# Kernel tuning notes

Measured on AMD Instinct MI355X. Metric: run time of the kernel, lower is better.

## Reference

```python
import jax, jax.numpy as jnp
import numpy as np

C_Z = 128
C_HIDDEN = 32
N_HEAD = 4
HC = N_HEAD * C_HIDDEN  # 128
LN_EPS = 1e-5


def setup_inputs() -> dict:
    key = jax.random.key(0)
    ks = jax.random.split(key, 8)
    b, n = 1, 256
    s = 1.0 / np.sqrt(C_Z)
    return {
        "z_ij": jax.random.normal(ks[0], (b, n, n, C_Z), dtype=jnp.float32),
        "ln_gamma": jnp.ones((C_Z,), dtype=jnp.float32),
        "ln_beta": jnp.zeros((C_Z,), dtype=jnp.float32),
        "Wq": jax.random.normal(ks[1], (C_Z, HC), dtype=jnp.float32) * s,
        "Wk": jax.random.normal(ks[2], (C_Z, HC), dtype=jnp.float32) * s,
        "Wv": jax.random.normal(ks[3], (C_Z, HC), dtype=jnp.float32) * s,
        "Wb": jax.random.normal(ks[4], (C_Z, N_HEAD), dtype=jnp.float32) * s,
        "Wg": jax.random.normal(ks[5], (C_Z, HC), dtype=jnp.float32) * s,
        "Wout": jax.random.normal(ks[6], (HC, C_Z), dtype=jnp.float32) * (1.0 / np.sqrt(HC)),
    }


def reference(z_ij, ln_gamma, ln_beta, Wq, Wk, Wv, Wb, Wg, Wout):
    b, n, _, _ = z_ij.shape
    # LayerNorm over c_z
    mu = jnp.mean(z_ij, axis=-1, keepdims=True)
    var = jnp.var(z_ij, axis=-1, keepdims=True)
    z = (z_ij - mu) * jax.lax.rsqrt(var + LN_EPS) * ln_gamma + ln_beta

    def heads(x):  # [b,i,j,hc] -> [b,i,j,h,d]
        return x.reshape(b, n, n, N_HEAD, C_HIDDEN)

    q = heads(z @ Wq)
    k = heads(z @ Wk)
    v = heads(z @ Wv)
    bias = z @ Wb                      # [b,i,j,h]
    g = jax.nn.sigmoid(heads(z @ Wg))  # [b,i,j,h,d]

    scores = jnp.einsum('bijhd,bikhd->bijkh', q, k) / np.sqrt(C_HIDDEN)
    scores = scores + bias[:, None]    # bias[b, j, k, h] broadcast over i
    a = jax.nn.softmax(scores, axis=-2)  # over k
    o = jnp.einsum('bijkh,bikhd->bijhd', a, v)
    o = (g * o).reshape(b, n, n, HC)
    return o @ Wout
```

## Files before the change

kernel.cpp:

```cpp
#include <hip/hip_runtime.h>

typedef _Float16 f16x8 __attribute__((ext_vector_type(8)));
typedef _Float16 f16x2 __attribute__((ext_vector_type(2)));
typedef float f32x4 __attribute__((ext_vector_type(4)));
typedef int i32x4 __attribute__((ext_vector_type(4)));

#define MFMA16(a, b, c) __builtin_amdgcn_mfma_f32_16x16x32_f16(a, b, c, 0, 0, 0)

#define NROW 65536
#define SEGB 16777216ull
#define LOG2E 1.4426950408889634f

__global__ __launch_bounds__(256) void k_ln(
    const float* __restrict__ z, const float* __restrict__ gamma,
    const float* __restrict__ beta, const float* __restrict__ Wb,
    const float* __restrict__ Wq, const float* __restrict__ Wk,
    const float* __restrict__ Wv, const float* __restrict__ Wg,
    const float* __restrict__ Wout,
    _Float16* __restrict__ zln, float* __restrict__ biasT,
    _Float16* __restrict__ WtAll)
{
  __shared__ _Float16 sw[32 * 136];
  int bid = blockIdx.x;
  if (bid < 16384) {
    int lane = threadIdx.x & 63;
    int w = threadIdx.x >> 6;
    int row = bid * 4 + w;
    float2 v = ((const float2*)(z + (size_t)row * 128))[lane];
    float s = v.x + v.y;
    #pragma unroll
    for (int m = 1; m < 64; m <<= 1) s += __shfl_xor(s, m);
    float mu = s * 0.0078125f;
    float dx = v.x - mu, dy = v.y - mu;
    float q = dx * dx + dy * dy;
    #pragma unroll
    for (int m = 1; m < 64; m <<= 1) q += __shfl_xor(q, m);
    float rs = rsqrtf(q * 0.0078125f + 1e-5f);
    float2 g2 = ((const float2*)gamma)[lane];
    float2 b2 = ((const float2*)beta)[lane];
    float y0 = dx * rs * g2.x + b2.x;
    float y1 = dy * rs * g2.y + b2.y;
    f16x2 pr; pr.x = (_Float16)y0; pr.y = (_Float16)y1;
    *(f16x2*)(zln + (size_t)row * 128 + 2 * lane) = pr;
    float4 wb0 = ((const float4*)Wb)[2 * lane];
    float4 wb1 = ((const float4*)Wb)[2 * lane + 1];
    float pb0 = y0 * wb0.x + y1 * wb1.x;
    float pb1 = y0 * wb0.y + y1 * wb1.y;
    float pb2 = y0 * wb0.z + y1 * wb1.z;
    float pb3 = y0 * wb0.w + y1 * wb1.w;
    #pragma unroll
    for (int m = 1; m < 64; m <<= 1) {
      pb0 += __shfl_xor(pb0, m);
      pb1 += __shfl_xor(pb1, m);
      pb2 += __shfl_xor(pb2, m);
      pb3 += __shfl_xor(pb3, m);
    }
    if (lane == 0) {
      int tix = ((row & 255) << 8) + (row >> 8);
      biasT[tix] = pb0 * LOG2E;
      biasT[NROW + tix] = pb1 * LOG2E;
      biasT[2 * NROW + tix] = pb2 * LOG2E;
      biasT[3 * NROW + tix] = pb3 * LOG2E;
    }
  } else {
    int t = bid - 16384;
    int mat = t >> 2, n0 = (t & 3) * 32;
    const float* src = (mat == 0) ? Wq : (mat == 1) ? Wk : (mat == 2) ? Wv
                       : (mat == 3) ? Wg : Wout;
    _Float16* dst = WtAll + mat * 16384;
    for (int it = 0; it < 16; ++it) {
      int e = threadIdx.x + it * 256;
      int c = e >> 5, j = e & 31;
      sw[j * 136 + c] = (_Float16)src[c * 128 + n0 + j];
    }
    __syncthreads();
    for (int it = 0; it < 2; ++it) {
      int ch = threadIdx.x + it * 256;
      int n = ch >> 4, k8 = (ch & 15) * 8;
      *(int4*)(dst + (n0 + n) * 128 + k8) = *(const int4*)&sw[n * 136 + k8];
    }
  }
}

__global__ __launch_bounds__(256) void k_proj(
    const _Float16* __restrict__ A, const _Float16* __restrict__ WtAll,
    _Float16* __restrict__ Qb, _Float16* __restrict__ Kb,
    _Float16* __restrict__ Vb, _Float16* __restrict__ Gb)
{
  __shared__ _Float16 sA[128 * 136];
  __shared__ _Float16 sB[128 * 136];
  int e = blockIdx.x;
  int by = (e >> 3) & 3;
  int xb = ((e >> 5) << 3) | (e & 7);
  int m0 = xb * 128;
  const _Float16* Bt = WtAll + by * 16384;
  _Float16* outp = (by == 0) ? Qb : (by == 1) ? Kb : (by == 2) ? Vb : Gb;
  int tid = threadIdx.x;
  for (int it = 0; it < 8; ++it) {
    int ch = tid + it * 256;
    int r = ch >> 4, c8 = (ch & 15) * 8;
    *(int4*)&sA[r * 136 + c8] = *(const int4*)(A + (size_t)(m0 + r) * 128 + c8);
    *(int4*)&sB[r * 136 + c8] = *(const int4*)(Bt + r * 128 + c8);
  }
  __syncthreads();
  int lane = tid & 63, w = tid >> 6;
  int mw = (w >> 1) * 64, nw = (w & 1) * 64;
  int lr = lane & 15, lg = lane >> 4;
  f32x4 z4 = {0.f, 0.f, 0.f, 0.f};
  f32x4 acc[4][4];
  #pragma unroll
  for (int mt = 0; mt < 4; ++mt)
    #pragma unroll
    for (int nt = 0; nt < 4; ++nt) acc[mt][nt] = z4;
  #pragma unroll
  for (int k0 = 0; k0 < 128; k0 += 32) {
    f16x8 af[4], bf[4];
    #pragma unroll
    for (int mt = 0; mt < 4; ++mt)
      af[mt] = *(const f16x8*)&sA[(mw + mt * 16 + lr) * 136 + k0 + lg * 8];
    #pragma unroll
    for (int nt = 0; nt < 4; ++nt)
      bf[nt] = *(const f16x8*)&sB[(nw + nt * 16 + lr) * 136 + k0 + lg * 8];
    #pragma unroll
    for (int mt = 0; mt < 4; ++mt)
      #pragma unroll
      for (int nt = 0; nt < 4; ++nt)
        acc[mt][nt] = MFMA16(af[mt], bf[nt], acc[mt][nt]);
  }
  bool sig = (by == 3);
  #pragma unroll
  for (int mt = 0; mt < 4; ++mt)
    #pragma unroll
    for (int nt = 0; nt < 4; ++nt)
      #pragma unroll
      for (int r = 0; r < 4; ++r) {
        int row = m0 + mw + mt * 16 + lg * 4 + r;
        int col = nw + nt * 16 + lr;
        float v = acc[mt][nt][r];
        if (sig) v = 1.0f / (1.0f + __expf(-v));
        outp[(size_t)row * 128 + col] = (_Float16)v;
      }
}

__global__ __launch_bounds__(256) void k_attn(
    const _Float16* __restrict__ Qb, const _Float16* __restrict__ Kb,
    const _Float16* __restrict__ Vb, const _Float16* __restrict__ Gb,
    const float* __restrict__ biasT, _Float16* __restrict__ OG)
{
  __shared__ _Float16 sK[256 * 32];
  __shared__ _Float16 sV[32 * 256];
  int i = blockIdx.x, h = blockIdx.y;
  int tid = threadIdx.x;
  size_t base = ((size_t)i * 256) * 128 + h * 32;
  for (int it = 0; it < 4; ++it) {
    int ch = tid + it * 256;
    int r = ch >> 2, cx = ch & 3;
    int p = cx ^ ((r >> 1) & 3);
    *(int4*)&sK[r * 32 + p * 8] = *(const int4*)(Kb + base + (size_t)r * 128 + cx * 8);
  }
  for (int it = 0; it < 4; ++it) {
    int ch = tid + it * 256;
    int k = ch >> 2, d8 = (ch & 3) * 8;
    f16x8 tv = *(const f16x8*)(Vb + base + (size_t)k * 128 + d8);
    #pragma unroll
    for (int jj = 0; jj < 8; ++jj) {
      int d = d8 + jj;
      int p = (k >> 3) ^ (d & 7);
      sV[d * 256 + p * 8 + (k & 7)] = tv[jj];
    }
  }
  __syncthreads();
  int lane = tid & 63, w = tid >> 6;
  int lr = lane & 15, lg = lane >> 4;
  const float scale = 0.2550348858f;
  f32x4 z4 = {0.f, 0.f, 0.f, 0.f};
  int la = lr + ((lg & 1) << 5);
  int lb = la + 16;
  int hi = lg >> 1;
  for (int pass = 0; pass < 4; ++pass) {
    int jbase = pass * 64;
    int jg = jbase + (w << 4) + lr;
    f16x8 aq = *(const f16x8*)(Qb + base + (size_t)jg * 128 + lg * 8);
    f32x4 sacc[16];
    __builtin_amdgcn_s_setprio(1);
    #pragma unroll
    for (int kt = 0; kt < 16; ++kt) {
      int r = kt * 16 + lr;
      int p = lg ^ ((r >> 1) & 3);
      f16x8 bk = *(const f16x8*)&sK[r * 32 + p * 8];
      sacc[kt] = MFMA16(bk, aq, z4);
    }
    __builtin_amdgcn_s_setprio(0);
    const float* bp = biasT + ((size_t)h << 16) + ((lg * 4) << 8) + jg;
    float mx = -1e30f;
    #pragma unroll
    for (int kt = 0; kt < 16; ++kt) {
      const float* bb = bp + (kt << 12);
      float b0 = bb[0], b1 = bb[256], b2 = bb[512], b3 = bb[768];
      sacc[kt][0] = sacc[kt][0] * scale + b0;
      sacc[kt][1] = sacc[kt][1] * scale + b1;
      sacc[kt][2] = sacc[kt][2] * scale + b2;
      sacc[kt][3] = sacc[kt][3] * scale + b3;
      mx = fmaxf(mx, fmaxf(fmaxf(sacc[kt][0], sacc[kt][1]),
                           fmaxf(sacc[kt][2], sacc[kt][3])));
    }
    mx = fmaxf(mx, __shfl_xor(mx, 16));
    mx = fmaxf(mx, __shfl_xor(mx, 32));
    float sum = 0.f;
    int q16[16][2];
    #pragma unroll
    for (int kt = 0; kt < 16; ++kt) {
      float p0 = exp2f(sacc[kt][0] - mx);
      float p1 = exp2f(sacc[kt][1] - mx);
      float p2 = exp2f(sacc[kt][2] - mx);
      float p3 = exp2f(sacc[kt][3] - mx);
      sum += (p0 + p1) + (p2 + p3);
      f16x2 w01, w23;
      w01.x = (_Float16)p0; w01.y = (_Float16)p1;
      w23.x = (_Float16)p2; w23.y = (_Float16)p3;
      q16[kt][0] = __builtin_bit_cast(int, w01);
      q16[kt][1] = __builtin_bit_cast(int, w23);
    }
    sum += __shfl_xor(sum, 16);
    sum += __shfl_xor(sum, 32);
    float rinv = 1.0f / sum;
    float rr0 = __shfl(rinv, (lg << 2));
    float rr1 = __shfl(rinv, (lg << 2) + 1);
    float rr2 = __shfl(rinv, (lg << 2) + 2);
    float rr3 = __shfl(rinv, (lg << 2) + 3);
    f32x4 oacc[2] = {z4, z4};
    #pragma unroll
    for (int ks = 0; ks < 8; ++ks) {
      int a0 = __shfl(q16[2 * ks][0], la);
      int a1 = __shfl(q16[2 * ks][1], la);
      int c0 = __shfl(q16[2 * ks + 1][0], la);
      int c1 = __shfl(q16[2 * ks + 1][1], la);
      int b0 = __shfl(q16[2 * ks][0], lb);
      int b1 = __shfl(q16[2 * ks][1], lb);
      int d0 = __shfl(q16[2 * ks + 1][0], lb);
      int d1 = __shfl(q16[2 * ks + 1][1], lb);
      i32x4 wv;
      wv.x = hi ? c0 : a0;
      wv.y = hi ? c1 : a1;
      wv.z = hi ? d0 : b0;
      wv.w = hi ? d1 : b1;
      f16x8 ap = __builtin_bit_cast(f16x8, wv);
      __builtin_amdgcn_s_setprio(1);
      #pragma unroll
      for (int nt = 0; nt < 2; ++nt) {
        int d = nt * 16 + lr;
        int c = ks * 4 + lg;
        f16x8 bv = *(const f16x8*)&sV[d * 256 + (c ^ (d & 7)) * 8];
        oacc[nt] = MFMA16(ap, bv, oacc[nt]);
      }
      __builtin_amdgcn_s_setprio(0);
    }
    float rrs[4] = {rr0, rr1, rr2, rr3};
    #pragma unroll
    for (int nt = 0; nt < 2; ++nt)
      #pragma unroll
      for (int r = 0; r < 4; ++r) {
        int j = jbase + (w << 4) + (lg << 2) + r;
        int d = nt * 16 + lr;
        size_t idx = base + (size_t)j * 128 + d;
        float g = (float)Gb[idx];
        OG[idx] = (_Float16)(oacc[nt][r] * rrs[r] * g);
      }
  }
}

__global__ __launch_bounds__(256) void k_outp(
    const _Float16* __restrict__ A, const _Float16* __restrict__ Bt,
    float* __restrict__ out)
{
  __shared__ _Float16 sA[128 * 136];
  __shared__ _Float16 sB[128 * 136];
  int m0 = blockIdx.x * 128;
  int tid = threadIdx.x;
  for (int it = 0; it < 8; ++it) {
    int ch = tid + it * 256;
    int r = ch >> 4, c8 = (ch & 15) * 8;
    *(int4*)&sA[r * 136 + c8] = *(const int4*)(A + (size_t)(m0 + r) * 128 + c8);
    *(int4*)&sB[r * 136 + c8] = *(const int4*)(Bt + r * 128 + c8);
  }
  __syncthreads();
  int lane = tid & 63, w = tid >> 6;
  int mw = (w >> 1) * 64, nw = (w & 1) * 64;
  int lr = lane & 15, lg = lane >> 4;
  f32x4 z4 = {0.f, 0.f, 0.f, 0.f};
  f32x4 acc[4][4];
  #pragma unroll
  for (int mt = 0; mt < 4; ++mt)
    #pragma unroll
    for (int nt = 0; nt < 4; ++nt) acc[mt][nt] = z4;
  #pragma unroll
  for (int k0 = 0; k0 < 128; k0 += 32) {
    f16x8 af[4], bf[4];
    #pragma unroll
    for (int mt = 0; mt < 4; ++mt)
      af[mt] = *(const f16x8*)&sA[(mw + mt * 16 + lr) * 136 + k0 + lg * 8];
    #pragma unroll
    for (int nt = 0; nt < 4; ++nt)
      bf[nt] = *(const f16x8*)&sB[(nw + nt * 16 + lr) * 136 + k0 + lg * 8];
    #pragma unroll
    for (int mt = 0; mt < 4; ++mt)
      #pragma unroll
      for (int nt = 0; nt < 4; ++nt)
        acc[mt][nt] = MFMA16(af[mt], bf[nt], acc[mt][nt]);
  }
  #pragma unroll
  for (int mt = 0; mt < 4; ++mt)
    #pragma unroll
    for (int nt = 0; nt < 4; ++nt)
      #pragma unroll
      for (int r = 0; r < 4; ++r) {
        int row = m0 + mw + mt * 16 + lg * 4 + r;
        int col = nw + nt * 16 + lr;
        out[(size_t)row * 128 + col] = acc[mt][nt][r];
      }
}

extern "C" void kernel_launch(void* const* d_in, const int* in_sizes, int n_in,
                              void* d_out, int out_size, void* d_ws, size_t ws_size,
                              hipStream_t stream) {
  (void)in_sizes; (void)n_in; (void)out_size; (void)ws_size;
  const float* z    = (const float*)d_in[0];
  const float* gam  = (const float*)d_in[1];
  const float* bet  = (const float*)d_in[2];
  const float* Wq   = (const float*)d_in[3];
  const float* Wk   = (const float*)d_in[4];
  const float* Wv   = (const float*)d_in[5];
  const float* Wb   = (const float*)d_in[6];
  const float* Wg   = (const float*)d_in[7];
  const float* Wout = (const float*)d_in[8];

  char* ws = (char*)d_ws;
  _Float16* zln   = (_Float16*)(ws);
  _Float16* Qb    = (_Float16*)(ws + SEGB);
  _Float16* Kb    = (_Float16*)(ws + SEGB * 2);
  _Float16* Vb    = (_Float16*)(ws + SEGB * 3);
  _Float16* Gb    = (_Float16*)(ws + SEGB * 4);
  float*    biasT = (float*)   (ws + SEGB * 5);
  _Float16* WtAll = (_Float16*)(ws + SEGB * 5 + 1048576);

  k_ln<<<16404, 256, 0, stream>>>(z, gam, bet, Wb, Wq, Wk, Wv, Wg, Wout,
                                  zln, biasT, WtAll);
  k_proj<<<2048, 256, 0, stream>>>(zln, WtAll, Qb, Kb, Vb, Gb);
  k_attn<<<dim3(256, 4), 256, 0, stream>>>(Qb, Kb, Vb, Gb, biasT, zln);
  k_outp<<<512, 256, 0, stream>>>(zln, WtAll + 4 * 16384, (float*)d_out);
}
```

Measured before the change: 215.0 us.

## Store bias untransposed for vector loads and interleave exp with PV MFMAs

The bias tensor is now written in natural row order, so the attention kernel reads four contiguous bias values per tile with one float4 load instead of four strided scalar loads. The softmax exponentials are also computed inside the PV MFMA loop rather than in a separate pass that materialised all sixteen packed probability pairs first. This cuts register pressure from the q16 array and lets transcendental work overlap with matrix instructions. The sum reduction still happens after the loop, so normalisation order is unchanged.

```diff
diff --git a/kernel.cpp b/kernel.cpp
--- a/kernel.cpp
+++ b/kernel.cpp
@@ -56,11 +56,10 @@
       pb3 += __shfl_xor(pb3, m);
     }
     if (lane == 0) {
-      int tix = ((row & 255) << 8) + (row >> 8);
-      biasT[tix] = pb0 * LOG2E;
-      biasT[NROW + tix] = pb1 * LOG2E;
-      biasT[2 * NROW + tix] = pb2 * LOG2E;
-      biasT[3 * NROW + tix] = pb3 * LOG2E;
+      biasT[row] = pb0 * LOG2E;
+      biasT[NROW + row] = pb1 * LOG2E;
+      biasT[2 * NROW + row] = pb2 * LOG2E;
+      biasT[3 * NROW + row] = pb3 * LOG2E;
     }
   } else {
     int t = bid - 16384;
@@ -191,35 +190,65 @@
       sacc[kt] = MFMA16(bk, aq, z4);
     }
     __builtin_amdgcn_s_setprio(0);
-    const float* bp = biasT + ((size_t)h << 16) + ((lg * 4) << 8) + jg;
+    const float* bp = biasT + ((size_t)h << 16) + ((size_t)jg << 8) + (lg << 2);
     float mx = -1e30f;
     #pragma unroll
     for (int kt = 0; kt < 16; ++kt) {
-      const float* bb = bp + (kt << 12);
-      float b0 = bb[0], b1 = bb[256], b2 = bb[512], b3 = bb[768];
-      sacc[kt][0] = sacc[kt][0] * scale + b0;
-      sacc[kt][1] = sacc[kt][1] * scale + b1;
-      sacc[kt][2] = sacc[kt][2] * scale + b2;
-      sacc[kt][3] = sacc[kt][3] * scale + b3;
+      float4 b4 = *(const float4*)(bp + kt * 16);
+      sacc[kt][0] = sacc[kt][0] * scale + b4.x;
+      sacc[kt][1] = sacc[kt][1] * scale + b4.y;
+      sacc[kt][2] = sacc[kt][2] * scale + b4.z;
+      sacc[kt][3] = sacc[kt][3] * scale + b4.w;
       mx = fmaxf(mx, fmaxf(fmaxf(sacc[kt][0], sacc[kt][1]),
                            fmaxf(sacc[kt][2], sacc[kt][3])));
     }
     mx = fmaxf(mx, __shfl_xor(mx, 16));
     mx = fmaxf(mx, __shfl_xor(mx, 32));
     float sum = 0.f;
-    int q16[16][2];
-    #pragma unroll
-    for (int kt = 0; kt < 16; ++kt) {
-      float p0 = exp2f(sacc[kt][0] - mx);
-      float p1 = exp2f(sacc[kt][1] - mx);
-      float p2 = exp2f(sacc[kt][2] - mx);
-      float p3 = exp2f(sacc[kt][3] - mx);
-      sum += (p0 + p1) + (p2 + p3);
-      f16x2 w01, w23;
-      w01.x = (_Float16)p0; w01.y = (_Float16)p1;
-      w23.x = (_Float16)p2; w23.y = (_Float16)p3;
-      q16[kt][0] = __builtin_bit_cast(int, w01);
-      q16[kt][1] = __builtin_bit_cast(int, w23);
+    f32x4 oacc[2] = {z4, z4};
+    #pragma unroll
+    for (int ks = 0; ks < 8; ++ks) {
+      float p0 = exp2f(sacc[2 * ks][0] - mx);
+      float p1 = exp2f(sacc[2 * ks][1] - mx);
+      float p2 = exp2f(sacc[2 * ks][2] - mx);
+      float p3 = exp2f(sacc[2 * ks][3] - mx);
+      float p4 = exp2f(sacc[2 * ks + 1][0] - mx);
+      float p5 = exp2f(sacc[2 * ks + 1][1] - mx);
+      float p6 = exp2f(sacc[2 * ks + 1][2] - mx);
+      float p7 = exp2f(sacc[2 * ks + 1][3] - mx);
+      sum += ((p0 + p1) + (p2 + p3)) + ((p4 + p5) + (p6 + p7));
+      f16x2 wA0, wA1, wB0, wB1;
+      wA0.x = (_Float16)p0; wA0.y = (_Float16)p1;
+      wA1.x = (_Float16)p2; wA1.y = (_Float16)p3;
+      wB0.x = (_Float16)p4; wB0.y = (_Float16)p5;
+      wB1.x = (_Float16)p6; wB1.y = (_Float16)p7;
+      int A0 = __builtin_bit_cast(int, wA0);
+      int A1 = __builtin_bit_cast(int, wA1);
+      int B0 = __builtin_bit_cast(int, wB0);
+      int B1 = __builtin_bit_cast(int, wB1);
+      int a0 = __shfl(A0, la);
+      int a1 = __shfl(A1, la);
+      int c0 = __shfl(B0, la);
+      int c1 = __shfl(B1, la);
+      int b0 = __shfl(A0, lb);
+      int b1 = __shfl(A1, lb);
+      int d0 = __shfl(B0, lb);
+      int d1 = __shfl(B1, lb);
+      i32x4 wv;
+      wv.x = hi ? c0 : a0;
+      wv.y = hi ? c1 : a1;
+      wv.z = hi ? d0 : b0;
+      wv.w = hi ? d1 : b1;
+      f16x8 ap = __builtin_bit_cast(f16x8, wv);
+      __builtin_amdgcn_s_setprio(1);
+      #pragma unroll
+      for (int nt = 0; nt < 2; ++nt) {
+        int d = nt * 16 + lr;
+        int c = ks * 4 + lg;
+        f16x8 bv = *(const f16x8*)&sV[d * 256 + (c ^ (d & 7)) * 8];
+        oacc[nt] = MFMA16(ap, bv, oacc[nt]);
+      }
+      __builtin_amdgcn_s_setprio(0);
     }
     sum += __shfl_xor(sum, 16);
     sum += __shfl_xor(sum, 32);
@@ -228,33 +257,6 @@
     float rr1 = __shfl(rinv, (lg << 2) + 1);
     float rr2 = __shfl(rinv, (lg << 2) + 2);
     float rr3 = __shfl(rinv, (lg << 2) + 3);
-    f32x4 oacc[2] = {z4, z4};
-    #pragma unroll
-    for (int ks = 0; ks < 8; ++ks) {
-      int a0 = __shfl(q16[2 * ks][0], la);
-      int a1 = __shfl(q16[2 * ks][1], la);
-      int c0 = __shfl(q16[2 * ks + 1][0], la);
-      int c1 = __shfl(q16[2 * ks + 1][1], la);
-      int b0 = __shfl(q16[2 * ks][0], lb);
-      int b1 = __shfl(q16[2 * ks][1], lb);
-      int d0 = __shfl(q16[2 * ks + 1][0], lb);
-      int d1 = __shfl(q16[2 * ks + 1][1], lb);
-      i32x4 wv;
-      wv.x = hi ? c0 : a0;
-      wv.y = hi ? c1 : a1;
-      wv.z = hi ? d0 : b0;
-      wv.w = hi ? d1 : b1;
-      f16x8 ap = __builtin_bit_cast(f16x8, wv);
-      __builtin_amdgcn_s_setprio(1);
-      #pragma unroll
-      for (int nt = 0; nt < 2; ++nt) {
-        int d = nt * 16 + lr;
-        int c = ks * 4 + lg;
-        f16x8 bv = *(const f16x8*)&sV[d * 256 + (c ^ (d & 7)) * 8];
-        oacc[nt] = MFMA16(ap, bv, oacc[nt]);
-      }
-      __builtin_amdgcn_s_setprio(0);
-    }
     float rrs[4] = {rr0, rr1, rr2, rr3};
     #pragma unroll
     for (int nt = 0; nt < 2; ++nt)
```

Result: slower. 247.4 us (+15.1%).
